# Kernel tuning notes

Measured on AMD Instinct MI355X. Metric: run time of the kernel, lower is better.

The kernel has to match this reference:

```python
import jax, jax.numpy as jnp
import numpy as np

D = 64       # desc_dim
PD = 64      # pose_dim
NH = 4       # num_heads
PS = 5       # patch_size
B, N, H, W = 16, 1024, 256, 256


def setup_inputs() -> dict:
    key = jax.random.key(0)
    ks = jax.random.split(key, 16)
    s = 1.0 / np.sqrt(D)
    inp = {
        "desc_points": jax.random.normal(ks[0], (B, N, D), jnp.float32),
        "shared_feat_map": jax.random.normal(ks[1], (B, D, H, W), jnp.float32),
        "coords": jax.random.randint(ks[2], (B, N, 2), 0, H),
        "pose_embed": jax.random.normal(ks[3], (B, PD), jnp.float32),
        "Wq": jax.random.normal(ks[4], (D, D), jnp.float32) * s,
        "bq": jnp.zeros((D,), jnp.float32),
        "Wk": jax.random.normal(ks[5], (D, D), jnp.float32) * s,
        "bk": jnp.zeros((D,), jnp.float32),
        "Wv": jax.random.normal(ks[6], (D, D), jnp.float32) * s,
        "bv": jnp.zeros((D,), jnp.float32),
        "Wp": jax.random.normal(ks[7], (PD, D), jnp.float32) * s,
        "bp": jnp.zeros((D,), jnp.float32),
        "Wo": jax.random.normal(ks[8], (D, D), jnp.float32) * s,
        "bo": jnp.zeros((D,), jnp.float32),
    }
    return inp


def _patch_means(feat_map, coords):
    # feat_map: [B,C,H,W], coords: [B,N,2] int (y,x). Vectorized ROI mean-pool.
    pad = PS // 2
    padded = jnp.pad(feat_map, ((0, 0), (0, 0), (pad, pad), (pad, pad)))
    y = coords[..., 0]
    x = coords[..., 1]
    off = jnp.arange(PS)
    rows = y[:, :, None, None] + off[None, None, :, None]   # [B,N,PS,1]
    cols = x[:, :, None, None] + off[None, None, None, :]   # [B,N,1,PS]
    bidx = jnp.arange(feat_map.shape[0])[:, None, None, None]
    # advanced indexing: result [B,N,PS,PS,C]
    patches = padded[bidx, :, rows, cols]
    return patches.mean(axis=(2, 3))  # [B,N,C]


def reference(desc_points, shared_feat_map, coords, pose_embed,
              Wq, bq, Wk, bk, Wv, bv, Wp, bp, Wo, bo):
    b, n, c = desc_points.shape
    hd = c // NH
    patch_feats = _patch_means(shared_feat_map, coords)  # [B,N,C]

    q = (desc_points @ Wq + bq).reshape(b, n, NH, hd)
    k = (patch_feats @ Wk + bk).reshape(b, n, NH, hd)
    v = (patch_feats @ Wv + bv).reshape(b, n, NH, hd)

    scores = jnp.einsum('bnhd,bmhd->bhnm', q, k) / jnp.sqrt(jnp.float32(hd))
    probs = jax.nn.softmax(scores, axis=-1)
    attn = jnp.einsum('bhnm,bmhd->bnhd', probs, v).reshape(b, n, c)

    pose_mod = pose_embed @ Wp + bp               # [B,C]
    fused = attn * (1.0 + pose_mod[:, None, :])   # [B,N,C]
    return fused @ Wo + bo
```

## Files before the change

kernel.cpp:

```cpp
#include <hip/hip_runtime.h>
#include <cstdint>
#include <cstddef>

#define BB 16
#define NN 1024
#define DD 64
#define NHH 4
#define HDD 16
#define KSPL 8
#define CAP 64

#define OFF_Q   0
#define OFF_K   (OFF_Q + BB*NHH*NN*HDD)
#define OFF_V   (OFF_K + BB*NHH*NN*HDD)
#define OFF_L   (OFF_V + BB*NHH*NN*HDD)
#define OFF_AT  (OFF_L + KSPL*64*NN)
#define OFF_PM  (OFF_AT + (size_t)KSPL*64*NN*HDD)
#define OFF_PF  (OFF_PM + 1024)
#define OFF_CNT (OFF_PF + BB*NN*DD)
#define OFF_LST (OFF_CNT + BB*256)
#define NEED_FULL ((size_t)(OFF_LST + (size_t)BB*256*CAP) * 4)

#define SL 260

__global__ __launch_bounds__(256) void k_zero(
    float* __restrict__ pf, int* __restrict__ cnt)
{
    int bid = blockIdx.x, t = threadIdx.x;
    if (bid < 1024) {
        ((float4*)pf)[bid * 256 + t] = make_float4(0.f, 0.f, 0.f, 0.f);
    } else {
        int4* c4 = (int4*)cnt;
        #pragma unroll
        for (int j = 0; j < 4; ++j) c4[t * 4 + j] = make_int4(0, 0, 0, 0);
    }
}

__global__ __launch_bounds__(256) void k_bin(
    const int* __restrict__ coords, int* __restrict__ cnt, int* __restrict__ lst)
{
    int pid = blockIdx.x * 256 + threadIdx.x;
    int y = coords[pid * 2 + 0];
    int x = coords[pid * 2 + 1];
    int b = pid >> 10;
    int slot = atomicAdd(&cnt[b * 256 + y], 1);
    if (slot < CAP) lst[(b * 256 + y) * CAP + slot] = (pid << 8) | x;
}

__global__ __launch_bounds__(256) void k_thsum_scat(
    const float* __restrict__ fm,
    const int* __restrict__ cnt, const int* __restrict__ lst,
    float* __restrict__ pf)
{
    __shared__ float L[32 * SL];
    int t   = threadIdx.x;
    int bid = blockIdx.x;
    int b   = bid >> 9;
    int y   = (bid >> 1) & 255;
    int ch  = bid & 1;

    int w = t >> 6, l = t & 63;
    const float* src = fm + ((size_t)b << 22) + ((size_t)(ch * 32) << 16) + ((size_t)y << 8);
    #pragma unroll
    for (int i = 0; i < 8; ++i) {
        int c = w * 8 + i;
        float4 v = *(const float4*)(src + ((size_t)c << 16) + l * 4);
        float pz = __shfl_up(v.z, 1);
        float pw = __shfl_up(v.w, 1);
        float nx = __shfl_down(v.x, 1);
        float ny = __shfl_down(v.y, 1);
        if (l == 0)  { pz = 0.f; pw = 0.f; }
        if (l == 63) { nx = 0.f; ny = 0.f; }
        float s3 = v.x + v.y + v.z;
        float s4 = s3 + v.w;
        float4 hs;
        hs.x = pz + pw + s3;
        hs.y = pw + s4;
        hs.z = s4 + nx;
        hs.w = v.y + v.z + v.w + nx + ny;
        *(float4*)(&L[c * SL + 4 * l]) = hs;
    }
    __syncthreads();

    int c  = t & 31;
    int ps = t >> 5;
    float* pfc = pf + ch * 32 + c;
    #pragma unroll
    for (int dy = -2; dy <= 2; ++dy) {
        int yy = y + dy;
        if ((unsigned)yy < 256u) {
            int base = b * 256 + yy;
            int nc = cnt[base];
            if (nc > CAP) nc = CAP;
            for (int s0 = ps; s0 < nc; s0 += 8) {
                int e   = lst[base * CAP + s0];
                int pid = e >> 8;
                int x   = e & 255;
                atomicAdd(pfc + (size_t)pid * 64, L[c * SL + x]);
            }
        }
    }
}

__global__ __launch_bounds__(256) void k_pf_qkv_pf(
    const float* __restrict__ desc, const float* __restrict__ pf,
    const float* __restrict__ Wq, const float* __restrict__ bq,
    const float* __restrict__ Wk, const float* __restrict__ bk,
    const float* __restrict__ Wv, const float* __restrict__ bv,
    float* __restrict__ Q, float* __restrict__ K, float* __restrict__ V)
{
    int w   = threadIdx.x >> 6;
    int c   = threadIdx.x & 63;
    int pid = blockIdx.x * 4 + w;
    int b   = pid >> 10;
    int n   = pid & 1023;

    __shared__ float spf[4][64];
    __shared__ float sd[4][64];

    spf[w][c] = pf[(size_t)pid * 64 + c] * 0.04f;
    sd[w][c]  = desc[(size_t)pid * 64 + c];
    __syncthreads();

    float aq = bq[c], ak = bk[c], av = bv[c];
    #pragma unroll 8
    for (int i = 0; i < 64; ++i) {
        float xd = sd[w][i];
        float xp = spf[w][i];
        aq = fmaf(xd, Wq[i * 64 + c], aq);
        ak = fmaf(xp, Wk[i * 64 + c], ak);
        av = fmaf(xp, Wv[i * 64 + c], av);
    }
    int h = c >> 4, d = c & 15;
    size_t o = (((size_t)b * 4 + h) * 1024 + n) * 16 + d;
    Q[o] = aq; K[o] = ak; V[o] = av;
}

__global__ __launch_bounds__(256) void k_pf_qkv(
    const float* __restrict__ desc, const float* __restrict__ fm,
    const int* __restrict__ coords,
    const float* __restrict__ Wq, const float* __restrict__ bq,
    const float* __restrict__ Wk, const float* __restrict__ bk,
    const float* __restrict__ Wv, const float* __restrict__ bv,
    float* __restrict__ Q, float* __restrict__ K, float* __restrict__ V)
{
    int w   = threadIdx.x >> 6;
    int c   = threadIdx.x & 63;
    int pid = blockIdx.x * 4 + w;
    int b   = pid >> 10;
    int n   = pid & 1023;

    __shared__ float spf[4][64];
    __shared__ float sd[4][64];

    int y = coords[pid * 2 + 0];
    int x = coords[pid * 2 + 1];

    const float* fmc = fm + ((size_t)(b * 64 + c) << 16);
    float s = 0.f;
    #pragma unroll
    for (int dy = -2; dy <= 2; ++dy) {
        int yy = y + dy;
        if ((unsigned)yy < 256u) {
            const float* row = fmc + yy * 256;
            #pragma unroll
            for (int dx = -2; dx <= 2; ++dx) {
                int xx = x + dx;
                if ((unsigned)xx < 256u) s += row[xx];
            }
        }
    }
    spf[w][c] = s * 0.04f;
    sd[w][c]  = desc[(size_t)pid * 64 + c];
    __syncthreads();

    float aq = bq[c], ak = bk[c], av = bv[c];
    #pragma unroll 8
    for (int i = 0; i < 64; ++i) {
        float xd = sd[w][i];
        float xp = spf[w][i];
        aq = fmaf(xd, Wq[i * 64 + c], aq);
        ak = fmaf(xp, Wk[i * 64 + c], ak);
        av = fmaf(xp, Wv[i * 64 + c], av);
    }
    int h = c >> 4, d = c & 15;
    size_t o = (((size_t)b * 4 + h) * 1024 + n) * 16 + d;
    Q[o] = aq; K[o] = ak; V[o] = av;
}

__global__ __launch_bounds__(64) void k_pose(
    const float* __restrict__ pe, const float* __restrict__ Wp,
    const float* __restrict__ bp, float* __restrict__ pm1)
{
    int b = blockIdx.x, c = threadIdx.x;
    __shared__ float sp[64];
    sp[c] = pe[b * 64 + c];
    __syncthreads();
    float acc = bp[c];
    #pragma unroll 8
    for (int i = 0; i < 64; ++i) acc = fmaf(sp[i], Wp[i * 64 + c], acc);
    pm1[b * 64 + c] = 1.f + acc;
}

__global__ __launch_bounds__(256, 2) void k_attn3(
    const float* __restrict__ Q, const float* __restrict__ K,
    const float* __restrict__ V,
    float* __restrict__ lpart, float* __restrict__ apart)
{
    int s  = blockIdx.x & 7;
    int bh = blockIdx.x >> 3;
    int t  = threadIdx.x;
    int b  = bh >> 2, h = bh & 3;

    const float4* Kb = ((const float4*)K) + ((size_t)bh << 12) + ((size_t)s << 9);
    const float4* Vb = ((const float4*)V) + ((size_t)bh << 12) + ((size_t)s << 9);

    float4 q[4][4];
    float4 A[4][4];
    float  l[4];
    #pragma unroll
    for (int i = 0; i < 4; ++i) {
        const float4* qp = ((const float4*)Q) + (((size_t)bh << 10) + t + 256 * i) * 4;
        #pragma unroll
        for (int j = 0; j < 4; ++j) { q[i][j] = qp[j]; A[i][j] = make_float4(0.f,0.f,0.f,0.f); }
        l[i] = 0.f;
    }

    for (int m = 0; m < 128; ++m) {
        float4 ka = Kb[m*4+0], kb = Kb[m*4+1], kc = Kb[m*4+2], kd = Kb[m*4+3];
        float4 va = Vb[m*4+0], vb = Vb[m*4+1], vc = Vb[m*4+2], vd = Vb[m*4+3];
        #pragma unroll
        for (int i = 0; i < 4; ++i) {
            float sc = q[i][0].x*ka.x + q[i][0].y*ka.y + q[i][0].z*ka.z + q[i][0].w*ka.w
                     + q[i][1].x*kb.x + q[i][1].y*kb.y + q[i][1].z*kb.z + q[i][1].w*kb.w
                     + q[i][2].x*kc.x + q[i][2].y*kc.y + q[i][2].z*kc.z + q[i][2].w*kc.w
                     + q[i][3].x*kd.x + q[i][3].y*kd.y + q[i][3].z*kd.z + q[i][3].w*kd.w;
            float p = __expf(sc * 0.25f);
            l[i] += p;
            A[i][0].x = fmaf(p, va.x, A[i][0].x); A[i][0].y = fmaf(p, va.y, A[i][0].y);
            A[i][0].z = fmaf(p, va.z, A[i][0].z); A[i][0].w = fmaf(p, va.w, A[i][0].w);
            A[i][1].x = fmaf(p, vb.x, A[i][1].x); A[i][1].y = fmaf(p, vb.y, A[i][1].y);
            A[i][1].z = fmaf(p, vb.z, A[i][1].z); A[i][1].w = fmaf(p, vb.w, A[i][1].w);
            A[i][2].x = fmaf(p, vc.x, A[i][2].x); A[i][2].y = fmaf(p, vc.y, A[i][2].y);
            A[i][2].z = fmaf(p, vc.z, A[i][2].z); A[i][2].w = fmaf(p, vc.w, A[i][2].w);
            A[i][3].x = fmaf(p, vd.x, A[i][3].x); A[i][3].y = fmaf(p, vd.y, A[i][3].y);
            A[i][3].z = fmaf(p, vd.z, A[i][3].z); A[i][3].w = fmaf(p, vd.w, A[i][3].w);
        }
    }

    #pragma unroll
    for (int i = 0; i < 4; ++i) {
        int n = t + 256 * i;
        lpart[(size_t)(s * 64 + bh) * 1024 + n] = l[i];
        float4* ap = (float4*)apart + ((((size_t)s * 16 + b) * 1024 + n) * 16) + h * 4;
        ap[0] = A[i][0]; ap[1] = A[i][1]; ap[2] = A[i][2]; ap[3] = A[i][3];
    }
}

__global__ __launch_bounds__(256) void k_out(
    const float* __restrict__ lpart, const float* __restrict__ apart,
    const float* __restrict__ pm1, const float* __restrict__ Wo,
    const float* __restrict__ bo, float* __restrict__ out)
{
    int w   = threadIdx.x >> 6;
    int c   = threadIdx.x & 63;
    int pid = blockIdx.x * 4 + w;
    int b   = pid >> 10;
    int n   = pid & 1023;
    int h   = c >> 4;
    int bh  = b * 4 + h;

    __shared__ float sf[4][64];

    float a = 0.f, ls = 0.f;
    #pragma unroll
    for (int s = 0; s < KSPL; ++s) {
        a  += apart[(((size_t)s * 16 + b) * 1024 + n) * 64 + c];
        ls += lpart[(size_t)(s * 64 + bh) * 1024 + n];
    }
    sf[w][c] = (a / ls) * pm1[b * 64 + c];
    __syncthreads();

    float acc = bo[c];
    #pragma unroll 8
    for (int i = 0; i < 64; ++i) acc = fmaf(sf[w][i], Wo[i * 64 + c], acc);
    out[(size_t)pid * 64 + c] = acc;
}

extern "C" void kernel_launch(void* const* d_in, const int* in_sizes, int n_in,
                              void* d_out, int out_size, void* d_ws, size_t ws_size,
                              hipStream_t stream)
{
    const float* desc = (const float*)d_in[0];
    const float* fm   = (const float*)d_in[1];
    const int*   crd  = (const int*)  d_in[2];
    const float* pe   = (const float*)d_in[3];
    const float* Wq   = (const float*)d_in[4];
    const float* bq   = (const float*)d_in[5];
    const float* Wk   = (const float*)d_in[6];
    const float* bk   = (const float*)d_in[7];
    const float* Wv   = (const float*)d_in[8];
    const float* bv   = (const float*)d_in[9];
    const float* Wp   = (const float*)d_in[10];
    const float* bp   = (const float*)d_in[11];
    const float* Wo   = (const float*)d_in[12];
    const float* bo   = (const float*)d_in[13];
    float* out = (float*)d_out;

    float* ws    = (float*)d_ws;
    float* Qb    = ws + OFF_Q;
    float* Kb    = ws + OFF_K;
    float* Vb    = ws + OFF_V;
    float* lpart = ws + OFF_L;
    float* apart = ws + OFF_AT;
    float* pm1   = ws + OFF_PM;
    float* pfb   = ws + OFF_PF;
    int*   cnt   = (int*)(ws + OFF_CNT);
    int*   lst   = (int*)(ws + OFF_LST);

    if (ws_size >= NEED_FULL) {
        hipLaunchKernelGGL(k_zero, dim3(1025), dim3(256), 0, stream, pfb, cnt);
        hipLaunchKernelGGL(k_bin, dim3(BB * NN / 256), dim3(256), 0, stream, crd, cnt, lst);
        hipLaunchKernelGGL(k_thsum_scat, dim3(BB * 256 * 2), dim3(256), 0, stream,
                           fm, cnt, lst, pfb);
        hipLaunchKernelGGL(k_pf_qkv_pf, dim3(BB * NN / 4), dim3(256), 0, stream,
                           desc, pfb, Wq, bq, Wk, bk, Wv, bv, Qb, Kb, Vb);
    } else {
        hipLaunchKernelGGL(k_pf_qkv, dim3(BB * NN / 4), dim3(256), 0, stream,
                           desc, fm, crd, Wq, bq, Wk, bk, Wv, bv, Qb, Kb, Vb);
    }
    hipLaunchKernelGGL(k_pose, dim3(BB), dim3(64), 0, stream, pe, Wp, bp, pm1);
    hipLaunchKernelGGL(k_attn3, dim3(64 * KSPL), dim3(256), 0, stream,
                       Qb, Kb, Vb, lpart, apart);
    hipLaunchKernelGGL(k_out, dim3(BB * NN / 4), dim3(256), 0, stream,
                       lpart, apart, pm1, Wo, bo, out);
}
```

Before: 537.2 us.

## Replace atomic patch scatter with per-row partial slots and restructure attention split

The patch-sum stage no longer zeroes a buffer and scatters with float atomics. Each row band now writes its horizontal sums into a dedicated per-point slot (five slots per point), and the QKV kernel sums the valid slots itself. The attention kernel changes from eight key splits with four queries per thread to one query per thread with two key halves per block. The halves are reduced in shared memory, normalised and multiplied by the pose term in place, which removes the large partial buffers and the separate reduction in the output kernel. The cost is a five-times-larger partial-patch buffer and less per-thread query reuse of each loaded K/V row.

```diff
diff --git a/kernel.cpp b/kernel.cpp
--- a/kernel.cpp
+++ b/kernel.cpp
@@ -7,33 +7,28 @@
 #define DD 64
 #define NHH 4
 #define HDD 16
-#define KSPL 8
 #define CAP 64
 
 #define OFF_Q   0
 #define OFF_K   (OFF_Q + BB*NHH*NN*HDD)
 #define OFF_V   (OFF_K + BB*NHH*NN*HDD)
-#define OFF_L   (OFF_V + BB*NHH*NN*HDD)
-#define OFF_AT  (OFF_L + KSPL*64*NN)
-#define OFF_PM  (OFF_AT + (size_t)KSPL*64*NN*HDD)
-#define OFF_PF  (OFF_PM + 1024)
-#define OFF_CNT (OFF_PF + BB*NN*DD)
+#define OFF_PM  (OFF_V + BB*NHH*NN*HDD)
+#define OFF_AP  (OFF_PM + 1024)
+#define OFF_CNT (OFF_AP + BB*NN*DD)
 #define OFF_LST (OFF_CNT + BB*256)
-#define NEED_FULL ((size_t)(OFF_LST + (size_t)BB*256*CAP) * 4)
+#define OFF_PP  (OFF_LST + BB*256*CAP)
+#define NEED_FULL ((size_t)(OFF_PP + (size_t)BB*NN*5*DD) * 4)
+#define NEED_MIN  ((size_t)OFF_CNT * 4)
 
 #define SL 260
 
-__global__ __launch_bounds__(256) void k_zero(
-    float* __restrict__ pf, int* __restrict__ cnt)
-{
-    int bid = blockIdx.x, t = threadIdx.x;
-    if (bid < 1024) {
-        ((float4*)pf)[bid * 256 + t] = make_float4(0.f, 0.f, 0.f, 0.f);
-    } else {
-        int4* c4 = (int4*)cnt;
-        #pragma unroll
-        for (int j = 0; j < 4; ++j) c4[t * 4 + j] = make_int4(0, 0, 0, 0);
-    }
+__global__ __launch_bounds__(256) void k_zero_cnt(int* __restrict__ cnt)
+{
+    int t = threadIdx.x;
+    int4 z = make_int4(0, 0, 0, 0);
+    int4* c4 = (int4*)cnt;
+    #pragma unroll
+    for (int j = 0; j < 4; ++j) c4[t * 4 + j] = z;
 }
 
 __global__ __launch_bounds__(256) void k_bin(
@@ -47,10 +42,10 @@
     if (slot < CAP) lst[(b * 256 + y) * CAP + slot] = (pid << 8) | x;
 }
 
-__global__ __launch_bounds__(256) void k_thsum_scat(
+__global__ __launch_bounds__(256) void k_thsum_part(
     const float* __restrict__ fm,
     const int* __restrict__ cnt, const int* __restrict__ lst,
-    float* __restrict__ pf)
+    float* __restrict__ pp)
 {
     __shared__ float L[32 * SL];
     int t   = threadIdx.x;
@@ -84,7 +79,6 @@
 
     int c  = t & 31;
     int ps = t >> 5;
-    float* pfc = pf + ch * 32 + c;
     #pragma unroll
     for (int dy = -2; dy <= 2; ++dy) {
         int yy = y + dy;
@@ -92,18 +86,20 @@
             int base = b * 256 + yy;
             int nc = cnt[base];
             if (nc > CAP) nc = CAP;
+            int slot = 2 - dy;
             for (int s0 = ps; s0 < nc; s0 += 8) {
                 int e   = lst[base * CAP + s0];
                 int pid = e >> 8;
                 int x   = e & 255;
-                atomicAdd(pfc + (size_t)pid * 64, L[c * SL + x]);
+                pp[(size_t)pid * 320 + slot * 64 + ch * 32 + c] = L[c * SL + x];
             }
         }
     }
 }
 
-__global__ __launch_bounds__(256) void k_pf_qkv_pf(
-    const float* __restrict__ desc, const float* __restrict__ pf,
+__global__ __launch_bounds__(256) void k_pf_qkv_part(
+    const float* __restrict__ desc, const float* __restrict__ pp,
+    const int* __restrict__ coords,
     const float* __restrict__ Wq, const float* __restrict__ bq,
     const float* __restrict__ Wk, const float* __restrict__ bk,
     const float* __restrict__ Wv, const float* __restrict__ bv,
@@ -118,7 +114,15 @@
     __shared__ float spf[4][64];
     __shared__ float sd[4][64];
 
-    spf[w][c] = pf[(size_t)pid * 64 + c] * 0.04f;
+    int y = coords[pid * 2 + 0];
+    const float* pprow = pp + (size_t)pid * 320 + c;
+    float s = 0.f;
+    #pragma unroll
+    for (int j = 0; j < 5; ++j) {
+        int yy = y + j - 2;
+        if ((unsigned)yy < 256u) s += pprow[j * 64];
+    }
+    spf[w][c] = s * 0.04f;
     sd[w][c]  = desc[(size_t)pid * 64 + c];
     __syncthreads();
 
@@ -202,83 +206,88 @@
     pm1[b * 64 + c] = 1.f + acc;
 }
 
-__global__ __launch_bounds__(256, 2) void k_attn3(
+__global__ __launch_bounds__(256) void k_attn_pm(
     const float* __restrict__ Q, const float* __restrict__ K,
-    const float* __restrict__ V,
-    float* __restrict__ lpart, float* __restrict__ apart)
-{
-    int s  = blockIdx.x & 7;
-    int bh = blockIdx.x >> 3;
+    const float* __restrict__ V, const float* __restrict__ pm1,
+    float* __restrict__ AP)
+{
+    int bh = blockIdx.x;
+    int qc = blockIdx.y;
+    int b  = bh >> 2, h = bh & 3;
     int t  = threadIdx.x;
-    int b  = bh >> 2, h = bh & 3;
-
-    const float4* Kb = ((const float4*)K) + ((size_t)bh << 12) + ((size_t)s << 9);
-    const float4* Vb = ((const float4*)V) + ((size_t)bh << 12) + ((size_t)s << 9);
-
-    float4 q[4][4];
-    float4 A[4][4];
-    float  l[4];
-    #pragma unroll
-    for (int i = 0; i < 4; ++i) {
-        const float4* qp = ((const float4*)Q) + (((size_t)bh << 10) + t + 256 * i) * 4;
-        #pragma unroll
-        for (int j = 0; j < 4; ++j) { q[i][j] = qp[j]; A[i][j] = make_float4(0.f,0.f,0.f,0.f); }
-        l[i] = 0.f;
-    }
-
-    for (int m = 0; m < 128; ++m) {
+    int ql = t & 127;
+    int kh = t >> 7;
+    int n  = qc * 128 + ql;
+
+    const float4* qp = (const float4*)Q + ((size_t)bh * 1024 + n) * 4;
+    float4 q0 = qp[0], q1 = qp[1], q2 = qp[2], q3 = qp[3];
+    const float4* Kb = (const float4*)K + ((size_t)bh * 1024 + (size_t)kh * 512) * 4;
+    const float4* Vb = (const float4*)V + ((size_t)bh * 1024 + (size_t)kh * 512) * 4;
+
+    float4 A0 = make_float4(0.f,0.f,0.f,0.f), A1 = A0, A2 = A0, A3 = A0;
+    float  l  = 0.f;
+
+    #pragma unroll 2
+    for (int m = 0; m < 512; ++m) {
         float4 ka = Kb[m*4+0], kb = Kb[m*4+1], kc = Kb[m*4+2], kd = Kb[m*4+3];
         float4 va = Vb[m*4+0], vb = Vb[m*4+1], vc = Vb[m*4+2], vd = Vb[m*4+3];
-        #pragma unroll
-        for (int i = 0; i < 4; ++i) {
-            float sc = q[i][0].x*ka.x + q[i][0].y*ka.y + q[i][0].z*ka.z + q[i][0].w*ka.w
-                     + q[i][1].x*kb.x + q[i][1].y*kb.y + q[i][1].z*kb.z + q[i][1].w*kb.w
-                     + q[i][2].x*kc.x + q[i][2].y*kc.y + q[i][2].z*kc.z + q[i][2].w*kc.w
-                     + q[i][3].x*kd.x + q[i][3].y*kd.y + q[i][3].z*kd.z + q[i][3].w*kd.w;
-            float p = __expf(sc * 0.25f);
-            l[i] += p;
-            A[i][0].x = fmaf(p, va.x, A[i][0].x); A[i][0].y = fmaf(p, va.y, A[i][0].y);
-            A[i][0].z = fmaf(p, va.z, A[i][0].z); A[i][0].w = fmaf(p, va.w, A[i][0].w);
-            A[i][1].x = fmaf(p, vb.x, A[i][1].x); A[i][1].y = fmaf(p, vb.y, A[i][1].y);
-            A[i][1].z = fmaf(p, vb.z, A[i][1].z); A[i][1].w = fmaf(p, vb.w, A[i][1].w);
-            A[i][2].x = fmaf(p, vc.x, A[i][2].x); A[i][2].y = fmaf(p, vc.y, A[i][2].y);
-            A[i][2].z = fmaf(p, vc.z, A[i][2].z); A[i][2].w = fmaf(p, vc.w, A[i][2].w);
-            A[i][3].x = fmaf(p, vd.x, A[i][3].x); A[i][3].y = fmaf(p, vd.y, A[i][3].y);
-            A[i][3].z = fmaf(p, vd.z, A[i][3].z); A[i][3].w = fmaf(p, vd.w, A[i][3].w);
-        }
-    }
-
-    #pragma unroll
-    for (int i = 0; i < 4; ++i) {
-        int n = t + 256 * i;
-        lpart[(size_t)(s * 64 + bh) * 1024 + n] = l[i];
-        float4* ap = (float4*)apart + ((((size_t)s * 16 + b) * 1024 + n) * 16) + h * 4;
-        ap[0] = A[i][0]; ap[1] = A[i][1]; ap[2] = A[i][2]; ap[3] = A[i][3];
-    }
-}
-
-__global__ __launch_bounds__(256) void k_out(
-    const float* __restrict__ lpart, const float* __restrict__ apart,
-    const float* __restrict__ pm1, const float* __restrict__ Wo,
+        float sc = q0.x*ka.x + q0.y*ka.y + q0.z*ka.z + q0.w*ka.w
+                 + q1.x*kb.x + q1.y*kb.y + q1.z*kb.z + q1.w*kb.w
+                 + q2.x*kc.x + q2.y*kc.y + q2.z*kc.z + q2.w*kc.w
+                 + q3.x*kd.x + q3.y*kd.y + q3.z*kd.z + q3.w*kd.w;
+        float p = __expf(sc * 0.25f);
+        l += p;
+        A0.x = fmaf(p, va.x, A0.x); A0.y = fmaf(p, va.y, A0.y);
+        A0.z = fmaf(p, va.z, A0.z); A0.w = fmaf(p, va.w, A0.w);
+        A1.x = fmaf(p, vb.x, A1.x); A1.y = fmaf(p, vb.y, A1.y);
+        A1.z = fmaf(p, vb.z, A1.z); A1.w = fmaf(p, vb.w, A1.w);
+        A2.x = fmaf(p, vc.x, A2.x); A2.y = fmaf(p, vc.y, A2.y);
+        A2.z = fmaf(p, vc.z, A2.z); A2.w = fmaf(p, vc.w, A2.w);
+        A3.x = fmaf(p, vd.x, A3.x); A3.y = fmaf(p, vd.y, A3.y);
+        A3.z = fmaf(p, vd.z, A3.z); A3.w = fmaf(p, vd.w, A3.w);
+    }
+
+    __shared__ float sA[128][16];
+    __shared__ float sL[128];
+    if (kh == 1) {
+        *(float4*)&sA[ql][0]  = A0; *(float4*)&sA[ql][4]  = A1;
+        *(float4*)&sA[ql][8]  = A2; *(float4*)&sA[ql][12] = A3;
+        sL[ql] = l;
+    }
+    __syncthreads();
+    if (kh == 0) {
+        float4 B0 = *(float4*)&sA[ql][0],  B1 = *(float4*)&sA[ql][4];
+        float4 B2 = *(float4*)&sA[ql][8],  B3 = *(float4*)&sA[ql][12];
+        float inv = 1.f / (l + sL[ql]);
+        const float4* pm = (const float4*)(pm1 + b * 64 + h * 16);
+        float4 p0 = pm[0], p1 = pm[1], p2 = pm[2], p3 = pm[3];
+        float* op = AP + ((size_t)b * 1024 + n) * 64 + h * 16;
+        float4 o;
+        o.x = (A0.x+B0.x)*inv*p0.x; o.y = (A0.y+B0.y)*inv*p0.y;
+        o.z = (A0.z+B0.z)*inv*p0.z; o.w = (A0.w+B0.w)*inv*p0.w;
+        *(float4*)(op + 0) = o;
+        o.x = (A1.x+B1.x)*inv*p1.x; o.y = (A1.y+B1.y)*inv*p1.y;
+        o.z = (A1.z+B1.z)*inv*p1.z; o.w = (A1.w+B1.w)*inv*p1.w;
+        *(float4*)(op + 4) = o;
+        o.x = (A2.x+B2.x)*inv*p2.x; o.y = (A2.y+B2.y)*inv*p2.y;
+        o.z = (A2.z+B2.z)*inv*p2.z; o.w = (A2.w+B2.w)*inv*p2.w;
+        *(float4*)(op + 8) = o;
+        o.x = (A3.x+B3.x)*inv*p3.x; o.y = (A3.y+B3.y)*inv*p3.y;
+        o.z = (A3.z+B3.z)*inv*p3.z; o.w = (A3.w+B3.w)*inv*p3.w;
+        *(float4*)(op + 12) = o;
+    }
+}
+
+__global__ __launch_bounds__(256) void k_out2(
+    const float* __restrict__ AP, const float* __restrict__ Wo,
     const float* __restrict__ bo, float* __restrict__ out)
 {
     int w   = threadIdx.x >> 6;
     int c   = threadIdx.x & 63;
     int pid = blockIdx.x * 4 + w;
-    int b   = pid >> 10;
-    int n   = pid & 1023;
-    int h   = c >> 4;
-    int bh  = b * 4 + h;
 
     __shared__ float sf[4][64];
-
-    float a = 0.f, ls = 0.f;
-    #pragma unroll
-    for (int s = 0; s < KSPL; ++s) {
-        a  += apart[(((size_t)s * 16 + b) * 1024 + n) * 64 + c];
-        ls += lpart[(size_t)(s * 64 + bh) * 1024 + n];
-    }
-    sf[w][c] = (a / ls) * pm1[b * 64 + c];
+    sf[w][c] = AP[(size_t)pid * 64 + c];
     __syncthreads();
 
     float acc = bo[c];
@@ -307,31 +316,30 @@
     const float* bo   = (const float*)d_in[13];
     float* out = (float*)d_out;
 
-    float* ws    = (float*)d_ws;
-    float* Qb    = ws + OFF_Q;
-    float* Kb    = ws + OFF_K;
-    float* Vb    = ws + OFF_V;
-    float* lpart = ws + OFF_L;
-    float* apart = ws + OFF_AT;
-    float* pm1   = ws + OFF_PM;
-    float* pfb   = ws + OFF_PF;
-    int*   cnt   = (int*)(ws + OFF_CNT);
-    int*   lst   = (int*)(ws + OFF_LST);
+    float* ws  = (float*)d_ws;
+    float* Qb  = ws + OFF_Q;
+    float* Kb  = ws + OFF_K;
+    float* Vb  = ws + OFF_V;
+    float* pm1 = ws + OFF_PM;
+    float* AP  = ws + OFF_AP;
+    int*   cnt = (int*)(ws + OFF_CNT);
+    int*   lst = (int*)(ws + OFF_LST);
+    float* pp  = ws + OFF_PP;
 
     if (ws_size >= NEED_FULL) {
-        hipLaunchKernelGGL(k_zero, dim3(1025), dim3(256), 0, stream, pfb, cnt);
+        hipLaunchKernelGGL(k_zero_cnt, dim3(1), dim3(256), 0, stream, cnt);
         hipLaunchKernelGGL(k_bin, dim3(BB * NN / 256), dim3(256), 0, stream, crd, cnt, lst);
-        hipLaunchKernelGGL(k_thsum_scat, dim3(BB * 256 * 2), dim3(256), 0, stream,
-                           fm, cnt, lst, pfb);
-        hipLaunchKernelGGL(k_pf_qkv_pf, dim3(BB * NN / 4), dim3(256), 0, stream,
-                           desc, pfb, Wq, bq, Wk, bk, Wv, bv, Qb, Kb, Vb);
+        hipLaunchKernelGGL(k_thsum_part, dim3(BB * 256 * 2), dim3(256), 0, stream,
+                           fm, cnt, lst, pp);
+        hipLaunchKernelGGL(k_pf_qkv_part, dim3(BB * NN / 4), dim3(256), 0, stream,
+                           desc, pp, crd, Wq, bq, Wk, bk, Wv, bv, Qb, Kb, Vb);
     } else {
         hipLaunchKernelGGL(k_pf_qkv, dim3(BB * NN / 4), dim3(256), 0, stream,
                            desc, fm, crd, Wq, bq, Wk, bk, Wv, bv, Qb, Kb, Vb);
     }
     hipLaunchKernelGGL(k_pose, dim3(BB), dim3(64), 0, stream, pe, Wp, bp, pm1);
-    hipLaunchKernelGGL(k_attn3, dim3(64 * KSPL), dim3(256), 0, stream,
-                       Qb, Kb, Vb, lpart, apart);
-    hipLaunchKernelGGL(k_out, dim3(BB * NN / 4), dim3(256), 0, stream,
-                       lpart, apart, pm1, Wo, bo, out);
-}
+    hipLaunchKernelGGL(k_attn_pm, dim3(64, 8), dim3(256), 0, stream,
+                       Qb, Kb, Vb, pm1, AP);
+    hipLaunchKernelGGL(k_out2, dim3(BB * NN / 4), dim3(256), 0, stream,
+                       AP, Wo, bo, out);
+}
```

Measured after the change: 755.9 us. 1.41x slower.
